# Kernel tuning notes

Measured on AMD Instinct MI355X. Metric: run time of the kernel, lower is better.

Reference implementation:

```python
import jax, jax.numpy as jnp
import numpy as np

B, HW, N = 4, 65536, 48
NEAR, FAR = 0.1, 10.0


def setup_inputs() -> dict:
    key = jax.random.key(0)
    k1, k2, k3 = jax.random.split(key, 3)
    rgb = jax.random.uniform(k1, (B, HW, N, 3), dtype=jnp.float32)
    sigma = jax.random.uniform(k2, (B, HW, N, 1), dtype=jnp.float32)
    # sorted sample depths in [near, far] along each ray
    z = jax.random.uniform(k3, (B, HW, N), dtype=jnp.float32)
    z_vals = NEAR + (FAR - NEAR) * jnp.sort(z, axis=-1)
    return {"rgb": rgb, "sigma": sigma, "z_vals": z_vals}


def reference(rgb, sigma, z_vals):
    # distances between consecutive samples; last dist is a huge cap value
    dists = z_vals[..., 1:] - z_vals[..., :-1]                       # (B, HW, N-1)
    dists = jnp.concatenate(
        [dists, jnp.full_like(dists[..., :1], 1e10)], axis=-1)      # (B, HW, N)
    alpha = 1.0 - jnp.exp(-sigma[..., 0] * dists)                    # (B, HW, N)
    # transmittance: exclusive cumulative product of (1 - alpha)
    T = jnp.cumprod(1.0 - alpha + 1e-10, axis=-1)
    T = jnp.concatenate([jnp.ones_like(T[..., :1]), T[..., :-1]], axis=-1)
    weights = alpha * T                                              # (B, HW, N)
    rgb_map = jnp.einsum('bns,bnsc->bnc', weights, rgb)              # (B, HW, 3)
    depth_map = jnp.sum(weights * z_vals, axis=-1)                   # (B, HW)
    return rgb_map, depth_map
```

## Files before the change

### kernel.cpp

```cpp
#include <hip/hip_runtime.h>

#define N_SAMP 48
#define TPR 4
#define SPT (N_SAMP / TPR)

__global__ __launch_bounds__(256) void volrender_kernel(
    const float4* __restrict__ rgb4,
    const float4* __restrict__ sigma4,
    const float4* __restrict__ z4,
    const float*  __restrict__ zf,
    float* __restrict__ out_rgb,
    float* __restrict__ out_depth,
    int n_rays)
{
    const int tid = blockIdx.x * blockDim.x + threadIdx.x;
    const int ray = tid >> 2;
    const int q   = tid & 3;
    if (ray >= n_rays) return;

    float zloc[SPT];
    float4* zv = reinterpret_cast<float4*>(zloc);
    const size_t zbase = (size_t)ray * 12 + q * 3;
#pragma unroll
    for (int k = 0; k < 3; ++k) zv[k] = z4[zbase + k];

    float znext = 0.0f;
    if (q < 3) znext = zf[(size_t)ray * N_SAMP + q * SPT + SPT];

    float sloc[SPT];
    float4* sv = reinterpret_cast<float4*>(sloc);
#pragma unroll
    for (int k = 0; k < 3; ++k) sv[k] = sigma4[zbase + k];

    float rloc[SPT * 3];
    float4* rv = reinterpret_cast<float4*>(rloc);
    const size_t rbase = (size_t)ray * 36 + q * 9;
#pragma unroll
    for (int k = 0; k < 9; ++k) rv[k] = rgb4[rbase + k];

    float T = 1.0f;
    float ar = 0.0f, ag = 0.0f, ab = 0.0f, ad = 0.0f;
#pragma unroll
    for (int j = 0; j < SPT; ++j) {
        const float zn   = (j < SPT - 1) ? zloc[j + 1] : znext;
        const bool  last = (j == SPT - 1);
        float dist  = (last && q == TPR - 1) ? 1e10f : (zn - zloc[j]);
        float alpha = 1.0f - __expf(-sloc[j] * dist);
        float w     = alpha * T;
        T *= (1.0f - alpha + 1e-10f);
        ar = fmaf(w, rloc[3 * j + 0], ar);
        ag = fmaf(w, rloc[3 * j + 1], ag);
        ab = fmaf(w, rloc[3 * j + 2], ab);
        ad = fmaf(w, zloc[j], ad);
    }

    const int lane = threadIdx.x & 63;
    const int base = lane & ~3;
    const float P  = T;
    const float P0 = __shfl(P, base + 0);
    const float P1 = __shfl(P, base + 1);
    const float P2 = __shfl(P, base + 2);
    float Tpre = 1.0f;
    if (q > 0) Tpre *= P0;
    if (q > 1) Tpre *= P1;
    if (q > 2) Tpre *= P2;

    ar *= Tpre; ag *= Tpre; ab *= Tpre; ad *= Tpre;

    ar += __shfl_xor(ar, 1); ag += __shfl_xor(ag, 1);
    ab += __shfl_xor(ab, 1); ad += __shfl_xor(ad, 1);
    ar += __shfl_xor(ar, 2); ag += __shfl_xor(ag, 2);
    ab += __shfl_xor(ab, 2); ad += __shfl_xor(ad, 2);

    if (q == 0) {
        out_rgb[(size_t)ray * 3 + 0] = ar;
        out_rgb[(size_t)ray * 3 + 1] = ag;
        out_rgb[(size_t)ray * 3 + 2] = ab;
        out_depth[ray] = ad;
    }
}

extern "C" void kernel_launch(void* const* d_in, const int* in_sizes, int n_in,
                              void* d_out, int out_size, void* d_ws, size_t ws_size,
                              hipStream_t stream) {
    const float4* rgb4   = (const float4*)d_in[0];
    const float4* sigma4 = (const float4*)d_in[1];
    const float4* z4     = (const float4*)d_in[2];
    const float*  zf     = (const float*)d_in[2];

    const int n_rays = in_sizes[2] / N_SAMP;

    float* out_rgb   = (float*)d_out;
    float* out_depth = out_rgb + (size_t)n_rays * 3;

    const int block     = 256;
    const int n_threads = n_rays * TPR;
    const int grid      = (n_threads + block - 1) / block;
    hipLaunchKernelGGL(volrender_kernel, dim3(grid), dim3(block), 0, stream,
                       rgb4, sigma4, z4, zf, out_rgb, out_depth, n_rays);
}
```

Before: 282.1 us.

## Stage ray data through shared memory with coalesced loads and shuffle-based znext

Each block now cooperatively loads its rays' z, sigma and rgb into LDS with fully coalesced float4 loads, then each thread reads its strided slice from LDS. Before, each thread issued strided float4 loads from global memory. The extra scalar global read for the next segment's first depth is replaced by a wave shuffle. This adds about 60KB of LDS per block and a barrier, which may limit occupancy and cause LDS bank conflicts on the strided per-thread reads. The staging loads also have no bounds guard for a partial final block.

```diff
diff --git a/kernel.cpp b/kernel.cpp
--- a/kernel.cpp
+++ b/kernel.cpp
@@ -3,40 +3,60 @@
 #define N_SAMP 48
 #define TPR 4
 #define SPT (N_SAMP / TPR)
+#define RPB 64
+#define BLOCK (RPB * TPR)
 
-__global__ __launch_bounds__(256) void volrender_kernel(
+__global__ __launch_bounds__(BLOCK) void volrender_kernel(
     const float4* __restrict__ rgb4,
     const float4* __restrict__ sigma4,
     const float4* __restrict__ z4,
-    const float*  __restrict__ zf,
     float* __restrict__ out_rgb,
     float* __restrict__ out_depth,
     int n_rays)
 {
-    const int tid = blockIdx.x * blockDim.x + threadIdx.x;
-    const int ray = tid >> 2;
-    const int q   = tid & 3;
-    if (ray >= n_rays) return;
+    __shared__ float4 z_s[RPB * 12];
+    __shared__ float4 s_s[RPB * 12];
+    __shared__ float4 r_s[RPB * 36];
+
+    const int t         = threadIdx.x;
+    const int block_ray = blockIdx.x * RPB;
+
+    {
+        const size_t zb = (size_t)block_ray * 12;
+#pragma unroll
+        for (int k = 0; k < 3; ++k)
+            z_s[k * BLOCK + t] = z4[zb + (size_t)k * BLOCK + t];
+#pragma unroll
+        for (int k = 0; k < 3; ++k)
+            s_s[k * BLOCK + t] = sigma4[zb + (size_t)k * BLOCK + t];
+        const size_t rb = (size_t)block_ray * 36;
+#pragma unroll
+        for (int k = 0; k < 9; ++k)
+            r_s[k * BLOCK + t] = rgb4[rb + (size_t)k * BLOCK + t];
+    }
+    __syncthreads();
+
+    const int rl  = t >> 2;
+    const int q   = t & 3;
+    const int ray = block_ray + rl;
 
     float zloc[SPT];
     float4* zv = reinterpret_cast<float4*>(zloc);
-    const size_t zbase = (size_t)ray * 12 + q * 3;
 #pragma unroll
-    for (int k = 0; k < 3; ++k) zv[k] = z4[zbase + k];
-
-    float znext = 0.0f;
-    if (q < 3) znext = zf[(size_t)ray * N_SAMP + q * SPT + SPT];
+    for (int k = 0; k < 3; ++k) zv[k] = z_s[rl * 12 + q * 3 + k];
 
     float sloc[SPT];
     float4* sv = reinterpret_cast<float4*>(sloc);
 #pragma unroll
-    for (int k = 0; k < 3; ++k) sv[k] = sigma4[zbase + k];
+    for (int k = 0; k < 3; ++k) sv[k] = s_s[rl * 12 + q * 3 + k];
 
     float rloc[SPT * 3];
     float4* rv = reinterpret_cast<float4*>(rloc);
-    const size_t rbase = (size_t)ray * 36 + q * 9;
 #pragma unroll
-    for (int k = 0; k < 9; ++k) rv[k] = rgb4[rbase + k];
+    for (int k = 0; k < 9; ++k) rv[k] = r_s[rl * 36 + q * 9 + k];
+
+    const int lane  = threadIdx.x & 63;
+    const float znext = __shfl(zloc[0], (lane + 1) & 63);
 
     float T = 1.0f;
     float ar = 0.0f, ag = 0.0f, ab = 0.0f, ad = 0.0f;
@@ -54,12 +74,11 @@
         ad = fmaf(w, zloc[j], ad);
     }
 
-    const int lane = threadIdx.x & 63;
-    const int base = lane & ~3;
-    const float P  = T;
-    const float P0 = __shfl(P, base + 0);
-    const float P1 = __shfl(P, base + 1);
-    const float P2 = __shfl(P, base + 2);
+    const int  base = lane & ~3;
+    const float P   = T;
+    const float P0  = __shfl(P, base + 0);
+    const float P1  = __shfl(P, base + 1);
+    const float P2  = __shfl(P, base + 2);
     float Tpre = 1.0f;
     if (q > 0) Tpre *= P0;
     if (q > 1) Tpre *= P1;
@@ -72,7 +91,7 @@
     ar += __shfl_xor(ar, 2); ag += __shfl_xor(ag, 2);
     ab += __shfl_xor(ab, 2); ad += __shfl_xor(ad, 2);
 
-    if (q == 0) {
+    if (q == 0 && ray < n_rays) {
         out_rgb[(size_t)ray * 3 + 0] = ar;
         out_rgb[(size_t)ray * 3 + 1] = ag;
         out_rgb[(size_t)ray * 3 + 2] = ab;
@@ -86,16 +105,13 @@
     const float4* rgb4   = (const float4*)d_in[0];
     const float4* sigma4 = (const float4*)d_in[1];
     const float4* z4     = (const float4*)d_in[2];
-    const float*  zf     = (const float*)d_in[2];
 
     const int n_rays = in_sizes[2] / N_SAMP;
 
     float* out_rgb   = (float*)d_out;
     float* out_depth = out_rgb + (size_t)n_rays * 3;
 
-    const int block     = 256;
-    const int n_threads = n_rays * TPR;
-    const int grid      = (n_threads + block - 1) / block;
-    hipLaunchKernelGGL(volrender_kernel, dim3(grid), dim3(block), 0, stream,
-                       rgb4, sigma4, z4, zf, out_rgb, out_depth, n_rays);
+    const int grid = (n_rays + RPB - 1) / RPB;
+    hipLaunchKernelGGL(volrender_kernel, dim3(grid), dim3(BLOCK), 0, stream,
+                       rgb4, sigma4, z4, out_rgb, out_depth, n_rays);
 }
```

New measurement: 273.1 us. 1.03x faster.
